# Performance work log

Hardware: AMD Instinct MI355X
Metric: run time of the kernel (lower is better)

## Reference

```python
import jax, jax.numpy as jnp
import numpy as np

V, E, ENC, D, A = 10000, 512, 2048, 512, 512  # vocab, embed, encoder_dim, decoder_dim, attention_dim
B, L, T = 64, 49, 20


def setup_inputs() -> dict:
    key = jax.random.key(0)
    ks = jax.random.split(key, 20)
    s = lambda k, shape, fan: jax.random.normal(k, shape, jnp.float32) / np.sqrt(fan)
    return {
        "encoder_out": jax.random.normal(ks[0], (B, L, ENC), jnp.float32),
        "captions": jax.random.randint(ks[1], (B, T), 0, V),
        "emb_table": s(ks[2], (V, E), E),
        "W_enc_att": s(ks[3], (ENC, A), ENC), "b_enc_att": jnp.zeros((A,), jnp.float32),
        "W_dec_att": s(ks[4], (D, A), D), "b_dec_att": jnp.zeros((A,), jnp.float32),
        "w_full": s(ks[5], (A,), A), "b_full": jnp.zeros((), jnp.float32),
        "W_ih": s(ks[6], (4 * D, E + ENC), E + ENC), "b_ih": jnp.zeros((4 * D,), jnp.float32),
        "W_hh": s(ks[7], (4 * D, D), D), "b_hh": jnp.zeros((4 * D,), jnp.float32),
        "W_init_h": s(ks[8], (ENC, D), ENC), "b_init_h": jnp.zeros((D,), jnp.float32),
        "W_init_c": s(ks[9], (ENC, D), ENC), "b_init_c": jnp.zeros((D,), jnp.float32),
        "W_out": s(ks[10], (D, V), D), "b_out": jnp.zeros((V,), jnp.float32),
    }


def _decoder(encoder_out, captions, emb_table, W_enc_att, b_enc_att, W_dec_att,
             b_dec_att, w_full, b_full, W_ih, b_ih, W_hh, b_hh,
             W_init_h, b_init_h, W_init_c, b_init_c, W_out, b_out):
    # init hidden/cell from mean encoder features
    mean_enc = encoder_out.mean(axis=1)                      # (B, ENC)
    h = mean_enc @ W_init_h + b_init_h                        # (B, D)
    c = mean_enc @ W_init_c + b_init_c
    # precompute encoder projection for additive attention (shared across steps)
    enc_proj = jnp.einsum('ble,ea->bla', encoder_out, W_enc_att) + b_enc_att  # (B, L, A)
    embeddings = emb_table[captions]                          # (B, T, E)
    emb_seq = jnp.swapaxes(embeddings, 0, 1)                  # (T, B, E)
    Dh = h.shape[-1]

    def step(carry, emb_t):
        h, c = carry
        # additive attention over L=49 locations
        dec_proj = h @ W_dec_att + b_dec_att                  # (B, A)
        att = jax.nn.relu(enc_proj + dec_proj[:, None, :])    # (B, L, A)
        scores = jnp.einsum('bla,a->bl', att, w_full) + b_full
        alpha = jax.nn.softmax(scores, axis=-1)               # (B, L)
        context = jnp.einsum('bl,ble->be', alpha, encoder_out)  # (B, ENC)
        # LSTMCell (PyTorch gate order: i, f, g, o)
        x = jnp.concatenate([emb_t, context], axis=1)         # (B, E+ENC)
        gates = x @ W_ih.T + b_ih + h @ W_hh.T + b_hh         # (B, 4D)
        i, f, g, o = jnp.split(gates, 4, axis=1)
        i, f, o = jax.nn.sigmoid(i), jax.nn.sigmoid(f), jax.nn.sigmoid(o)
        g = jnp.tanh(g)
        c_new = f * c + i * g
        h_new = o * jnp.tanh(c_new)
        # dropout is identity in eval mode
        logits_t = h_new @ W_out + b_out                      # (B, V)
        return (h_new, c_new), (logits_t, alpha)

    (_, _), (logits, alphas) = jax.lax.scan(step, (h, c), emb_seq)
    logits = jnp.swapaxes(logits, 0, 1)                       # (B, T, V)
    alphas = jnp.swapaxes(alphas, 0, 1)                       # (B, T, L)
    return logits, alphas


def reference(encoder_out, captions, emb_table, W_enc_att, b_enc_att, W_dec_att,
              b_dec_att, w_full, b_full, W_ih, b_ih, W_hh, b_hh,
              W_init_h, b_init_h, W_init_c, b_init_c, W_out, b_out):
    return _decoder(encoder_out, captions, emb_table, W_enc_att, b_enc_att,
                    W_dec_att, b_dec_att, w_full, b_full, W_ih, b_ih, W_hh, b_hh,
                    W_init_h, b_init_h, W_init_c, b_init_c, W_out, b_out)
```

## Files before the change

kernel.cpp:

```cpp
#include <hip/hip_runtime.h>
#include <hip/hip_bf16.h>

constexpr int NV   = 10000;
constexpr int NE   = 512;
constexpr int NENC = 2048;
constexpr int ND   = 512;
constexpr int NA   = 512;
constexpr int NB   = 64;
constexpr int NL   = 49;
constexpr int NT   = 20;
constexpr int KX   = NE + NENC + ND;
constexpr int KIH  = NE + NENC;

typedef short bfrag __attribute__((ext_vector_type(8)));
typedef float f32x4 __attribute__((ext_vector_type(4)));

__device__ __forceinline__ float us2f(unsigned short u) {
    union { unsigned int i; float f; } x; x.i = (unsigned int)u << 16; return x.f;
}
__device__ __forceinline__ unsigned short f2us(float f) {
    union { float f_; unsigned int u; } x; x.f_ = f;
    unsigned int r = (x.u + 0x7fffu + ((x.u >> 16) & 1u)) >> 16;
    return (unsigned short)r;
}

__launch_bounds__(256)
__global__ void k_mean(const float* __restrict__ enc, unsigned short* __restrict__ meanbf)
{
    const int b = blockIdx.x;
    const int e = blockIdx.y * 256 + threadIdx.x;
    const float* p = enc + (size_t)b * NL * NENC + e;
    float s = 0.f;
    #pragma unroll 7
    for (int l = 0; l < NL; ++l) s += p[(size_t)l * NENC];
    meanbf[(size_t)b * NENC + e] = f2us(s * (1.0f / NL));
}

__launch_bounds__(256)
__global__ void k_init_mfma(const unsigned short* __restrict__ meanbf,
                            const unsigned short* __restrict__ WicT,
                            const float* __restrict__ bh, const float* __restrict__ bc,
                            unsigned short* __restrict__ hbf, float* __restrict__ c)
{
    const int wave = threadIdx.x >> 6, lane = threadIdx.x & 63;
    const int m0 = wave * 16, n0 = blockIdx.x * 16;
    const int r = lane & 15, quad = lane >> 4;
    const unsigned short* ap = meanbf + (size_t)(m0 + r) * NENC + quad * 8;
    const unsigned short* bp = WicT   + (size_t)(n0 + r) * NENC + quad * 8;
    f32x4 acc = {0.f, 0.f, 0.f, 0.f};
    #pragma unroll 8
    for (int k = 0; k < NENC; k += 32) {
        bfrag a = *(const bfrag*)(ap + k);
        bfrag b = *(const bfrag*)(bp + k);
        acc = __builtin_amdgcn_mfma_f32_16x16x32_bf16(a, b, acc, 0, 0, 0);
    }
    const int n = n0 + r;
    const bool isC = n >= ND;
    const float bv = isC ? bc[n - ND] : bh[n];
    #pragma unroll
    for (int i = 0; i < 4; ++i) {
        int m = m0 + quad * 4 + i;
        float v = acc[i] + bv;
        if (isC) c[(size_t)m * ND + (n - ND)] = v;
        else     hbf[(size_t)m * ND + n] = f2us(v);
    }
}

__launch_bounds__(256)
__global__ void k_cvt(const float* __restrict__ src, unsigned short* __restrict__ dst, int n)
{
    int i = (blockIdx.x * 256 + threadIdx.x) * 4;
    if (i < n) {
        float4 v = *(const float4*)(src + i);
        dst[i + 0] = f2us(v.x); dst[i + 1] = f2us(v.y);
        dst[i + 2] = f2us(v.z); dst[i + 3] = f2us(v.w);
    }
}

__launch_bounds__(256)
__global__ void k_transpose(const float* __restrict__ src, unsigned short* __restrict__ dst,
                            int K, int N)
{
    __shared__ float t[32][33];
    const int nb = blockIdx.x * 32, kb = blockIdx.y * 32;
    const int tx = threadIdx.x & 31, ty = threadIdx.x >> 5;
    #pragma unroll
    for (int i = ty; i < 32; i += 8) {
        int n = nb + tx;
        t[i][tx] = (n < N) ? src[(size_t)(kb + i) * N + n] : 0.f;
    }
    __syncthreads();
    #pragma unroll
    for (int i = ty; i < 32; i += 8) {
        int n = nb + i;
        if (n < N) dst[(size_t)n * K + kb + tx] = f2us(t[tx][i]);
    }
}

__launch_bounds__(256)
__global__ void k_encproj_mfma(const unsigned short* __restrict__ encb,
                               const unsigned short* __restrict__ WeaT,
                               const float* __restrict__ bias,
                               unsigned short* __restrict__ epb)
{
    const int wave = threadIdx.x >> 6, lane = threadIdx.x & 63;
    const int ng = blockIdx.x & 7;
    const int mg = blockIdx.x >> 3;
    const int wm = wave >> 1, wn = wave & 1;
    const int m0 = mg * 64 + wm * 32;
    const int n0 = ng * 64 + wn * 32;
    const int r = lane & 15, quad = lane >> 4;
    const unsigned short* ap0 = encb + (size_t)(m0 + r) * NENC + quad * 8;
    const unsigned short* ap1 = ap0 + (size_t)16 * NENC;
    const unsigned short* bp0 = WeaT + (size_t)(n0 + r) * NENC + quad * 8;
    const unsigned short* bp1 = bp0 + (size_t)16 * NENC;
    f32x4 acc00 = {0.f,0.f,0.f,0.f}, acc01 = {0.f,0.f,0.f,0.f};
    f32x4 acc10 = {0.f,0.f,0.f,0.f}, acc11 = {0.f,0.f,0.f,0.f};
    #pragma unroll 4
    for (int k = 0; k < NENC; k += 32) {
        bfrag a0 = *(const bfrag*)(ap0 + k);
        bfrag a1 = *(const bfrag*)(ap1 + k);
        bfrag b0 = *(const bfrag*)(bp0 + k);
        bfrag b1 = *(const bfrag*)(bp1 + k);
        acc00 = __builtin_amdgcn_mfma_f32_16x16x32_bf16(a0, b0, acc00, 0, 0, 0);
        acc01 = __builtin_amdgcn_mfma_f32_16x16x32_bf16(a0, b1, acc01, 0, 0, 0);
        acc10 = __builtin_amdgcn_mfma_f32_16x16x32_bf16(a1, b0, acc10, 0, 0, 0);
        acc11 = __builtin_amdgcn_mfma_f32_16x16x32_bf16(a1, b1, acc11, 0, 0, 0);
    }
    const float bv0 = bias[n0 + r], bv1 = bias[n0 + 16 + r];
    #pragma unroll
    for (int i = 0; i < 4; ++i) {
        int ma = m0 + quad * 4 + i, mb = ma + 16;
        epb[(size_t)ma * NA + n0 + r]      = f2us(acc00[i] + bv0);
        epb[(size_t)ma * NA + n0 + 16 + r] = f2us(acc01[i] + bv1);
        epb[(size_t)mb * NA + n0 + r]      = f2us(acc10[i] + bv0);
        epb[(size_t)mb * NA + n0 + 16 + r] = f2us(acc11[i] + bv1);
    }
}

__launch_bounds__(512)
__global__ void k_att(int t,
                      const unsigned short* __restrict__ hbf,
                      const float* __restrict__ dpg,
                      const unsigned short* __restrict__ epb,
                      const unsigned short* __restrict__ encb,
                      const float* __restrict__ wf,
                      const float* __restrict__ bfs,
                      const float* __restrict__ embt,
                      const int* __restrict__ captions,
                      unsigned short* __restrict__ x,
                      float* __restrict__ alpha_out)
{
    __shared__ float dp[NA];
    __shared__ float al[64];
    const int b = blockIdx.x, tid = threadIdx.x;

    for (int d = tid; d < ND; d += 512)
        x[(size_t)b * KX + NE + NENC + d] = hbf[(size_t)b * ND + d];
    for (int a = tid; a < NA; a += 512)
        dp[a] = dpg[(size_t)b * NA + a];
    const int tok = captions[b * NT + t];
    for (int j = tid; j < NE; j += 512)
        x[(size_t)b * KX + j] = f2us(embt[(size_t)tok * NE + j]);
    __syncthreads();

    const int wave = tid >> 6, lane = tid & 63;
    const float bfull = bfs[0];
    for (int l = wave; l < NL; l += 8) {
        const unsigned short* ep = epb + ((size_t)b * NL + l) * NA;
        float s = 0.f;
        #pragma unroll
        for (int a = lane; a < NA; a += 64) {
            float v = us2f(ep[a]) + dp[a];
            v = v > 0.f ? v : 0.f;
            s = fmaf(v, wf[a], s);
        }
        #pragma unroll
        for (int off = 32; off > 0; off >>= 1) s += __shfl_down(s, off, 64);
        if (lane == 0) al[l] = s + bfull;
    }
    __syncthreads();

    if (tid < 64) {
        float v = (tid < NL) ? al[tid] : -1e30f;
        float m = v;
        #pragma unroll
        for (int off = 32; off > 0; off >>= 1) m = fmaxf(m, __shfl_xor(m, off, 64));
        float e = (tid < NL) ? expf(v - m) : 0.f;
        float s = e;
        #pragma unroll
        for (int off = 32; off > 0; off >>= 1) s += __shfl_xor(s, off, 64);
        float a = e / s;
        if (tid < NL) {
            al[tid] = a;
            alpha_out[((size_t)b * NT + t) * NL + tid] = a;
        }
    }
    __syncthreads();

    {
        const int e = tid * 4;
        const unsigned short* p = encb + (size_t)b * NL * NENC + e;
        float s0 = 0.f, s1 = 0.f, s2 = 0.f, s3 = 0.f;
        #pragma unroll 7
        for (int l = 0; l < NL; ++l) {
            ushort4 v = *(const ushort4*)(p + (size_t)l * NENC);
            float a = al[l];
            s0 = fmaf(a, us2f(v.x), s0);
            s1 = fmaf(a, us2f(v.y), s1);
            s2 = fmaf(a, us2f(v.z), s2);
            s3 = fmaf(a, us2f(v.w), s3);
        }
        unsigned short* xo = x + (size_t)b * KX + NE + e;
        xo[0] = f2us(s0); xo[1] = f2us(s1); xo[2] = f2us(s2); xo[3] = f2us(s3);
    }
}

__launch_bounds__(256)
__global__ void k_gates_lstm(const unsigned short* __restrict__ x,
                             const unsigned short* __restrict__ Wihb,
                             const unsigned short* __restrict__ Whhb,
                             const float* __restrict__ bih, const float* __restrict__ bhh,
                             unsigned short* __restrict__ hbf, float* __restrict__ c)
{
    __shared__ float part[3][4][16][16];
    const int wave = threadIdx.x >> 6, lane = threadIdx.x & 63;
    const int ng = blockIdx.x & 31, mt = blockIdx.x >> 5;
    const int m0 = mt * 16, n0 = ng * 16;
    const int r = lane & 15, quad = lane >> 4;
    const int k0 = wave * (KX / 4);
    const int k1 = k0 + (KX / 4);

    const unsigned short* ap = x + (size_t)(m0 + r) * KX + quad * 8;
    f32x4 acc[4] = {{0.f,0.f,0.f,0.f},{0.f,0.f,0.f,0.f},
                    {0.f,0.f,0.f,0.f},{0.f,0.f,0.f,0.f}};

    const int kiA = (k1 < KIH) ? k1 : KIH;
    #pragma unroll 4
    for (int k = k0; k < kiA; k += 32) {
        bfrag a = *(const bfrag*)(ap + k);
        #pragma unroll
        for (int g = 0; g < 4; ++g) {
            const unsigned short* bp = Wihb + (size_t)(g * ND + n0 + r) * KIH + quad * 8;
            bfrag b = *(const bfrag*)(bp + k);
            acc[g] = __builtin_amdgcn_mfma_f32_16x16x32_bf16(a, b, acc[g], 0, 0, 0);
        }
    }
    const int kiB = (k0 > KIH) ? k0 : KIH;
    #pragma unroll 4
    for (int k = kiB; k < k1; k += 32) {
        bfrag a = *(const bfrag*)(ap + k);
        #pragma unroll
        for (int g = 0; g < 4; ++g) {
            const unsigned short* bp = Whhb + (size_t)(g * ND + n0 + r) * ND + quad * 8;
            bfrag b = *(const bfrag*)(bp + (k - KIH));
            acc[g] = __builtin_amdgcn_mfma_f32_16x16x32_bf16(a, b, acc[g], 0, 0, 0);
        }
    }

    if (wave > 0) {
        #pragma unroll
        for (int g = 0; g < 4; ++g)
            #pragma unroll
            for (int i = 0; i < 4; ++i)
                part[wave - 1][g][quad * 4 + i][r] = acc[g][i];
    }
    __syncthreads();
    if (wave == 0) {
        #pragma unroll
        for (int g = 0; g < 4; ++g)
            #pragma unroll
            for (int i = 0; i < 4; ++i)
                acc[g][i] += part[0][g][quad * 4 + i][r]
                           + part[1][g][quad * 4 + i][r]
                           + part[2][g][quad * 4 + i][r];
        const int d = n0 + r;
        const float b0 = bih[d]        + bhh[d];
        const float b1 = bih[d + 512]  + bhh[d + 512];
        const float b2 = bih[d + 1024] + bhh[d + 1024];
        const float b3 = bih[d + 1536] + bhh[d + 1536];
        #pragma unroll
        for (int i = 0; i < 4; ++i) {
            const int m = m0 + quad * 4 + i;
            float gi = acc[0][i] + b0;
            float gf = acc[1][i] + b1;
            float gg = acc[2][i] + b2;
            float go = acc[3][i] + b3;
            float ig = 1.f / (1.f + expf(-gi));
            float fg = 1.f / (1.f + expf(-gf));
            float g  = tanhf(gg);
            float og = 1.f / (1.f + expf(-go));
            float cn = fg * c[(size_t)m * ND + d] + ig * g;
            float hn = og * tanhf(cn);
            c[(size_t)m * ND + d] = cn;
            hbf[(size_t)m * ND + d] = f2us(hn);
        }
    }
}

__launch_bounds__(256)
__global__ void k_logits_decproj(int t, int nlog,
                                 const unsigned short* __restrict__ hbf,
                                 const unsigned short* __restrict__ WoutT,
                                 const float* __restrict__ bout,
                                 float* __restrict__ out,
                                 const unsigned short* __restrict__ WdaT,
                                 const float* __restrict__ bda,
                                 float* __restrict__ dp)
{
    const int wave = threadIdx.x >> 6, lane = threadIdx.x & 63;
    const int r = lane & 15, quad = lane >> 4;
    const int m0 = wave * 16;
    if ((int)blockIdx.x < nlog) {
        const int n0 = blockIdx.x * 16;
        const unsigned short* ap = hbf + (size_t)(m0 + r) * ND + quad * 8;
        const unsigned short* bp = WoutT + (size_t)(n0 + r) * ND + quad * 8;
        f32x4 acc = {0.f, 0.f, 0.f, 0.f};
        #pragma unroll
        for (int k = 0; k < ND; k += 32) {
            bfrag a = *(const bfrag*)(ap + k);
            bfrag b = *(const bfrag*)(bp + k);
            acc = __builtin_amdgcn_mfma_f32_16x16x32_bf16(a, b, acc, 0, 0, 0);
        }
        const float bv = bout[n0 + r];
        #pragma unroll
        for (int i = 0; i < 4; ++i) {
            int m = m0 + quad * 4 + i;
            out[((size_t)m * NT + t) * NV + n0 + r] = acc[i] + bv;
        }
    } else {
        const int n0 = ((int)blockIdx.x - nlog) * 16;
        const unsigned short* ap = hbf + (size_t)(m0 + r) * ND + quad * 8;
        const unsigned short* bp = WdaT + (size_t)(n0 + r) * ND + quad * 8;
        f32x4 acc = {0.f, 0.f, 0.f, 0.f};
        #pragma unroll
        for (int k = 0; k < ND; k += 32) {
            bfrag a = *(const bfrag*)(ap + k);
            bfrag b = *(const bfrag*)(bp + k);
            acc = __builtin_amdgcn_mfma_f32_16x16x32_bf16(a, b, acc, 0, 0, 0);
        }
        const float bv = bda[n0 + r];
        #pragma unroll
        for (int i = 0; i < 4; ++i) {
            int m = m0 + quad * 4 + i;
            dp[(size_t)m * NA + n0 + r] = acc[i] + bv;
        }
    }
}

extern "C" void kernel_launch(void* const* d_in, const int* in_sizes, int n_in,
                              void* d_out, int out_size, void* d_ws, size_t ws_size,
                              hipStream_t stream) {
    const float* enc  = (const float*)d_in[0];
    const int*   caps = (const int*)d_in[1];
    const float* embt = (const float*)d_in[2];
    const float* Wea  = (const float*)d_in[3];
    const float* bea  = (const float*)d_in[4];
    const float* Wda  = (const float*)d_in[5];
    const float* bda  = (const float*)d_in[6];
    const float* wf   = (const float*)d_in[7];
    const float* bfs  = (const float*)d_in[8];
    const float* Wih  = (const float*)d_in[9];
    const float* bih  = (const float*)d_in[10];
    const float* Whh  = (const float*)d_in[11];
    const float* bhh  = (const float*)d_in[12];
    const float* Wh0  = (const float*)d_in[13];
    const float* bh0  = (const float*)d_in[14];
    const float* Wc0  = (const float*)d_in[15];
    const float* bc0  = (const float*)d_in[16];
    const float* Wout = (const float*)d_in[17];
    const float* bout = (const float*)d_in[18];

    float* out = (float*)d_out;
    float* alpha_out = out + (size_t)NB * NT * NV;

    char* w = (char*)d_ws;
    float* c     = (float*)w;                 w += (size_t)NB * ND * 4;
    float* dp    = (float*)w;                 w += (size_t)NB * NA * 4;
    unsigned short* meanbf = (unsigned short*)w; w += (size_t)NB * NENC * 2;
    unsigned short* hbf   = (unsigned short*)w; w += (size_t)NB * ND * 2;
    unsigned short* x     = (unsigned short*)w; w += (size_t)NB * KX * 2;
    unsigned short* epb   = (unsigned short*)w; w += (size_t)NB * NL * NA * 2;
    unsigned short* encb  = (unsigned short*)w; w += (size_t)NB * NL * NENC * 2;
    unsigned short* Wihb  = (unsigned short*)w; w += (size_t)4 * ND * KIH * 2;
    unsigned short* Whhb  = (unsigned short*)w; w += (size_t)4 * ND * ND * 2;
    unsigned short* WeaT  = (unsigned short*)w; w += (size_t)NA * NENC * 2;
    unsigned short* WdaT  = (unsigned short*)w; w += (size_t)NA * ND * 2;
    unsigned short* WoutT = (unsigned short*)w; w += (size_t)NV * ND * 2;
    unsigned short* WicT  = (unsigned short*)w; w += (size_t)2 * ND * NENC * 2;

    hipLaunchKernelGGL(k_mean, dim3(NB, NENC / 256), dim3(256), 0, stream, enc, meanbf);
    hipLaunchKernelGGL(k_transpose, dim3(ND / 32, NENC / 32), dim3(256), 0, stream,
                       Wh0, WicT, NENC, ND);
    hipLaunchKernelGGL(k_transpose, dim3(ND / 32, NENC / 32), dim3(256), 0, stream,
                       Wc0, WicT + (size_t)ND * NENC, NENC, ND);
    hipLaunchKernelGGL(k_init_mfma, dim3(2 * ND / 16), dim3(256), 0, stream,
                       meanbf, WicT, bh0, bc0, hbf, c);
    {
        int n = NB * NL * NENC;
        hipLaunchKernelGGL(k_cvt, dim3(n / 4 / 256), dim3(256), 0, stream, enc, encb, n);
    }
    {
        int n = 4 * ND * KIH;
        hipLaunchKernelGGL(k_cvt, dim3(n / 4 / 256), dim3(256), 0, stream, Wih, Wihb, n);
    }
    {
        int n = 4 * ND * ND;
        hipLaunchKernelGGL(k_cvt, dim3(n / 4 / 256), dim3(256), 0, stream, Whh, Whhb, n);
    }
    hipLaunchKernelGGL(k_transpose, dim3(NA / 32, NENC / 32), dim3(256), 0, stream,
                       Wea, WeaT, NENC, NA);
    hipLaunchKernelGGL(k_transpose, dim3(NA / 32, ND / 32), dim3(256), 0, stream,
                       Wda, WdaT, ND, NA);
    hipLaunchKernelGGL(k_transpose, dim3((NV + 31) / 32, ND / 32), dim3(256), 0, stream,
                       Wout, WoutT, ND, NV);
    hipLaunchKernelGGL(k_encproj_mfma, dim3((NB * NL / 64) * (NA / 64)), dim3(256), 0, stream,
                       encb, WeaT, bea, epb);
    hipLaunchKernelGGL(k_logits_decproj, dim3(32), dim3(256), 0, stream,
                       0, 0, hbf, WoutT, bout, out, WdaT, bda, dp);

    for (int t = 0; t < NT; ++t) {
        hipLaunchKernelGGL(k_att, dim3(NB), dim3(512), 0, stream,
                           t, hbf, dp, epb, encb, wf, bfs, embt, caps, x, alpha_out);
        hipLaunchKernelGGL(k_gates_lstm, dim3(128), dim3(256), 0, stream,
                           x, Wihb, Whhb, bih, bhh, hbf, c);
        hipLaunchKernelGGL(k_logits_decproj, dim3(NV / 16 + 32), dim3(256), 0, stream,
                           t, NV / 16, hbf, WoutT, bout, out, WdaT, bda, dp);
    }
}
```

Before: 1.105 ms.

## Fuse per-step decoder kernels into one persistent cooperative kernel with grid syncs

Replaces the 60 per-timestep kernel launches (attention, gates/LSTM, logits+decproj) with a single cooperative kernel of 256 blocks that loops over time steps and separates phases with grid.sync. Part of the logits work for step t-1 is overlapped with the attention phase of step t, and the gates reduction is split across 8 waves instead of 4. The encoder-projection block index is also remapped. This removes launch overhead and inter-kernel gaps, at the cost of grid-wide barriers and fewer blocks working on the logits GEMM.

```diff
diff --git a/kernel.cpp b/kernel.cpp
--- a/kernel.cpp
+++ b/kernel.cpp
@@ -1,5 +1,8 @@
 #include <hip/hip_runtime.h>
 #include <hip/hip_bf16.h>
+#include <hip/hip_cooperative_groups.h>
+
+namespace cg = cooperative_groups;
 
 constexpr int NV   = 10000;
 constexpr int NE   = 512;
@@ -103,9 +106,10 @@
                                const float* __restrict__ bias,
                                unsigned short* __restrict__ epb)
 {
+    const int j = (blockIdx.x & 7) * 49 + (blockIdx.x >> 3);
+    const int ng = j & 7;
+    const int mg = j >> 3;
     const int wave = threadIdx.x >> 6, lane = threadIdx.x & 63;
-    const int ng = blockIdx.x & 7;
-    const int mg = blockIdx.x >> 3;
     const int wm = wave >> 1, wn = wave & 1;
     const int m0 = mg * 64 + wm * 32;
     const int n0 = ng * 64 + wn * 32;
@@ -138,28 +142,18 @@
     }
 }
 
-__launch_bounds__(512)
-__global__ void k_att(int t,
-                      const unsigned short* __restrict__ hbf,
-                      const float* __restrict__ dpg,
-                      const unsigned short* __restrict__ epb,
-                      const unsigned short* __restrict__ encb,
-                      const float* __restrict__ wf,
-                      const float* __restrict__ bfs,
-                      const float* __restrict__ embt,
-                      const int* __restrict__ captions,
-                      unsigned short* __restrict__ x,
-                      float* __restrict__ alpha_out)
-{
-    __shared__ float dp[NA];
-    __shared__ float al[64];
-    const int b = blockIdx.x, tid = threadIdx.x;
-
+
+__device__ __forceinline__ void att_body(int t, int b, int tid,
+    const unsigned short* hbf, const float* dpg, const unsigned short* epb,
+    const unsigned short* encb, const float* wf, const float* bfs,
+    const float* embt, const int* caps, unsigned short* x, float* alpha_out,
+    float* dp , float* al )
+{
     for (int d = tid; d < ND; d += 512)
         x[(size_t)b * KX + NE + NENC + d] = hbf[(size_t)b * ND + d];
     for (int a = tid; a < NA; a += 512)
         dp[a] = dpg[(size_t)b * NA + a];
-    const int tok = captions[b * NT + t];
+    const int tok = caps[b * NT + t];
     for (int j = tid; j < NE; j += 512)
         x[(size_t)b * KX + j] = f2us(embt[(size_t)tok * NE + j]);
     __syncthreads();
@@ -216,22 +210,24 @@
     }
 }
 
-__launch_bounds__(256)
-__global__ void k_gates_lstm(const unsigned short* __restrict__ x,
-                             const unsigned short* __restrict__ Wihb,
-                             const unsigned short* __restrict__ Whhb,
-                             const float* __restrict__ bih, const float* __restrict__ bhh,
-                             unsigned short* __restrict__ hbf, float* __restrict__ c)
-{
-    __shared__ float part[3][4][16][16];
-    const int wave = threadIdx.x >> 6, lane = threadIdx.x & 63;
-    const int ng = blockIdx.x & 31, mt = blockIdx.x >> 5;
+__device__ __forceinline__ void gates_lstm_body(int bid, int wave, int lane,
+    const unsigned short* x, const unsigned short* Wihb, const unsigned short* Whhb,
+    const float* bih, const float* bhh, unsigned short* hbf, float* c,
+    float* part )
+{
+    const int ng = bid & 31, mt = bid >> 5;
     const int m0 = mt * 16, n0 = ng * 16;
     const int r = lane & 15, quad = lane >> 4;
-    const int k0 = wave * (KX / 4);
-    const int k1 = k0 + (KX / 4);
+    const int k0 = wave * (KX / 8), k1 = k0 + (KX / 8);
 
     const unsigned short* ap = x + (size_t)(m0 + r) * KX + quad * 8;
+    const unsigned short* bpih[4];
+    const unsigned short* bphh[4];
+    #pragma unroll
+    for (int g = 0; g < 4; ++g) {
+        bpih[g] = Wihb + (size_t)(g * ND + n0 + r) * KIH + quad * 8;
+        bphh[g] = Whhb + (size_t)(g * ND + n0 + r) * ND + quad * 8;
+    }
     f32x4 acc[4] = {{0.f,0.f,0.f,0.f},{0.f,0.f,0.f,0.f},
                     {0.f,0.f,0.f,0.f},{0.f,0.f,0.f,0.f}};
 
@@ -241,8 +237,7 @@
         bfrag a = *(const bfrag*)(ap + k);
         #pragma unroll
         for (int g = 0; g < 4; ++g) {
-            const unsigned short* bp = Wihb + (size_t)(g * ND + n0 + r) * KIH + quad * 8;
-            bfrag b = *(const bfrag*)(bp + k);
+            bfrag b = *(const bfrag*)(bpih[g] + k);
             acc[g] = __builtin_amdgcn_mfma_f32_16x16x32_bf16(a, b, acc[g], 0, 0, 0);
         }
     }
@@ -252,8 +247,7 @@
         bfrag a = *(const bfrag*)(ap + k);
         #pragma unroll
         for (int g = 0; g < 4; ++g) {
-            const unsigned short* bp = Whhb + (size_t)(g * ND + n0 + r) * ND + quad * 8;
-            bfrag b = *(const bfrag*)(bp + (k - KIH));
+            bfrag b = *(const bfrag*)(bphh[g] + (k - KIH));
             acc[g] = __builtin_amdgcn_mfma_f32_16x16x32_bf16(a, b, acc[g], 0, 0, 0);
         }
     }
@@ -263,17 +257,20 @@
         for (int g = 0; g < 4; ++g)
             #pragma unroll
             for (int i = 0; i < 4; ++i)
-                part[wave - 1][g][quad * 4 + i][r] = acc[g][i];
+                part[(((wave - 1) * 4 + g) * 16 + quad * 4 + i) * 16 + r] = acc[g][i];
     }
     __syncthreads();
     if (wave == 0) {
         #pragma unroll
         for (int g = 0; g < 4; ++g)
             #pragma unroll
-            for (int i = 0; i < 4; ++i)
-                acc[g][i] += part[0][g][quad * 4 + i][r]
-                           + part[1][g][quad * 4 + i][r]
-                           + part[2][g][quad * 4 + i][r];
+            for (int i = 0; i < 4; ++i) {
+                float v = acc[g][i];
+                #pragma unroll
+                for (int w = 0; w < 7; ++w)
+                    v += part[((w * 4 + g) * 16 + quad * 4 + i) * 16 + r];
+                acc[g][i] = v;
+            }
         const int d = n0 + r;
         const float b0 = bih[d]        + bhh[d];
         const float b1 = bih[d + 512]  + bhh[d + 512];
@@ -298,21 +295,16 @@
     }
 }
 
-__launch_bounds__(256)
-__global__ void k_logits_decproj(int t, int nlog,
-                                 const unsigned short* __restrict__ hbf,
-                                 const unsigned short* __restrict__ WoutT,
-                                 const float* __restrict__ bout,
-                                 float* __restrict__ out,
-                                 const unsigned short* __restrict__ WdaT,
-                                 const float* __restrict__ bda,
-                                 float* __restrict__ dp)
-{
-    const int wave = threadIdx.x >> 6, lane = threadIdx.x & 63;
+__device__ __forceinline__ void logits_tasks(int t, int lo, int hi,
+    int worker, int nworkers, int wave, int lane,
+    const unsigned short* hbf, const unsigned short* WoutT,
+    const float* bout, float* out)
+{
+    const int slot = wave >> 2, w4 = wave & 3;
     const int r = lane & 15, quad = lane >> 4;
-    const int m0 = wave * 16;
-    if ((int)blockIdx.x < nlog) {
-        const int n0 = blockIdx.x * 16;
+    const int m0 = w4 * 16;
+    for (int task = lo + worker * 2 + slot; task < hi; task += nworkers * 2) {
+        const int n0 = task * 16;
         const unsigned short* ap = hbf + (size_t)(m0 + r) * ND + quad * 8;
         const unsigned short* bp = WoutT + (size_t)(n0 + r) * ND + quad * 8;
         f32x4 acc = {0.f, 0.f, 0.f, 0.f};
@@ -328,24 +320,73 @@
             int m = m0 + quad * 4 + i;
             out[((size_t)m * NT + t) * NV + n0 + r] = acc[i] + bv;
         }
-    } else {
-        const int n0 = ((int)blockIdx.x - nlog) * 16;
-        const unsigned short* ap = hbf + (size_t)(m0 + r) * ND + quad * 8;
-        const unsigned short* bp = WdaT + (size_t)(n0 + r) * ND + quad * 8;
-        f32x4 acc = {0.f, 0.f, 0.f, 0.f};
-        #pragma unroll
-        for (int k = 0; k < ND; k += 32) {
-            bfrag a = *(const bfrag*)(ap + k);
-            bfrag b = *(const bfrag*)(bp + k);
-            acc = __builtin_amdgcn_mfma_f32_16x16x32_bf16(a, b, acc, 0, 0, 0);
-        }
-        const float bv = bda[n0 + r];
-        #pragma unroll
-        for (int i = 0; i < 4; ++i) {
-            int m = m0 + quad * 4 + i;
-            dp[(size_t)m * NA + n0 + r] = acc[i] + bv;
-        }
-    }
+    }
+}
+
+__device__ __forceinline__ void decproj_body(int bid, int wave, int lane,
+    const unsigned short* hbf, const unsigned short* WdaT,
+    const float* bda, float* dp)
+{
+    const int slot = wave >> 2, w4 = wave & 3;
+    const int tile = bid * 2 + slot;
+    const int n0 = tile * 16, m0 = w4 * 16;
+    const int r = lane & 15, quad = lane >> 4;
+    const unsigned short* ap = hbf + (size_t)(m0 + r) * ND + quad * 8;
+    const unsigned short* bp = WdaT + (size_t)(n0 + r) * ND + quad * 8;
+    f32x4 acc = {0.f, 0.f, 0.f, 0.f};
+    #pragma unroll
+    for (int k = 0; k < ND; k += 32) {
+        bfrag a = *(const bfrag*)(ap + k);
+        bfrag b = *(const bfrag*)(bp + k);
+        acc = __builtin_amdgcn_mfma_f32_16x16x32_bf16(a, b, acc, 0, 0, 0);
+    }
+    const float bv = bda[n0 + r];
+    #pragma unroll
+    for (int i = 0; i < 4; ++i) {
+        int m = m0 + quad * 4 + i;
+        dp[(size_t)m * NA + n0 + r] = acc[i] + bv;
+    }
+}
+
+__launch_bounds__(512)
+__global__ void k_loop(unsigned short* hbf, float* c, float* dp, unsigned short* x,
+                       const unsigned short* epb, const unsigned short* encb,
+                       const unsigned short* Wihb, const unsigned short* Whhb,
+                       const unsigned short* WdaT, const unsigned short* WoutT,
+                       const float* wf, const float* bfs, const float* embt,
+                       const int* caps, const float* bih, const float* bhh,
+                       const float* bda, const float* bout,
+                       float* out, float* alpha_out)
+{
+    __shared__ float smem[7 * 4 * 16 * 16];
+    cg::grid_group grid = cg::this_grid();
+    const int bid = blockIdx.x, tid = threadIdx.x;
+    const int wave = tid >> 6, lane = tid & 63;
+
+    if (bid < 16) decproj_body(bid, wave, lane, hbf, WdaT, bda, dp);
+    grid.sync();
+
+    for (int t = 0; t < NT; ++t) {
+        if (bid < 64)
+            att_body(t, bid, tid, hbf, dp, epb, encb, wf, bfs, embt, caps,
+                     x, alpha_out, smem, smem + 512);
+        else if (t > 0)
+            logits_tasks(t - 1, 384, 625, bid - 64, 192, wave, lane,
+                         hbf, WoutT, bout, out);
+        grid.sync();
+
+        if (bid < 128)
+            gates_lstm_body(bid, wave, lane, x, Wihb, Whhb, bih, bhh, hbf, c, smem);
+        grid.sync();
+
+        if (bid < 16)
+            decproj_body(bid, wave, lane, hbf, WdaT, bda, dp);
+        else if (bid >= 64)
+            logits_tasks(t, 0, 384, bid - 64, 192, wave, lane,
+                         hbf, WoutT, bout, out);
+        grid.sync();
+    }
+    logits_tasks(NT - 1, 384, 625, bid, 256, wave, lane, hbf, WoutT, bout, out);
 }
 
 extern "C" void kernel_launch(void* const* d_in, const int* in_sizes, int n_in,
@@ -416,15 +457,12 @@
                        Wout, WoutT, ND, NV);
     hipLaunchKernelGGL(k_encproj_mfma, dim3((NB * NL / 64) * (NA / 64)), dim3(256), 0, stream,
                        encb, WeaT, bea, epb);
-    hipLaunchKernelGGL(k_logits_decproj, dim3(32), dim3(256), 0, stream,
-                       0, 0, hbf, WoutT, bout, out, WdaT, bda, dp);
-
-    for (int t = 0; t < NT; ++t) {
-        hipLaunchKernelGGL(k_att, dim3(NB), dim3(512), 0, stream,
-                           t, hbf, dp, epb, encb, wf, bfs, embt, caps, x, alpha_out);
-        hipLaunchKernelGGL(k_gates_lstm, dim3(128), dim3(256), 0, stream,
-                           x, Wihb, Whhb, bih, bhh, hbf, c);
-        hipLaunchKernelGGL(k_logits_decproj, dim3(NV / 16 + 32), dim3(256), 0, stream,
-                           t, NV / 16, hbf, WoutT, bout, out, WdaT, bda, dp);
-    }
-}
+
+    {
+        void* args[] = { &hbf, &c, &dp, &x, &epb, &encb, &Wihb, &Whhb,
+                         &WdaT, &WoutT, &wf, &bfs, &embt, &caps,
+                         &bih, &bhh, &bda, &bout, &out, &alpha_out };
+        hipLaunchCooperativeKernel((const void*)k_loop, dim3(256), dim3(512),
+                                   args, 0, stream);
+    }
+}
```

Measured after the change: 2.813 ms. 155% more time.
